# Optimization experiments

Hardware: AMD Instinct MI355X
Metric: run time of the kernel (lower is better)

Reference implementation:

```python
import jax, jax.numpy as jnp
import numpy as np

NUM_SAMPLES = 512
FG_FRACTION = 0.25
MAX_POS = int(NUM_SAMPLES * FG_FRACTION)  # 128
THRESHOLDS = np.array([0.0, 0.5, 0.5], dtype=np.float32)
INDICATORS = np.array([-3, -1, -2, 1], dtype=np.int32)


def _make_boxes(key, shape, scale):
    # random valid boxes: sorted corner pairs in [0, scale)
    y = jnp.sort(jax.random.uniform(key, shape[:-1] + (2,)) * scale, axis=-1)
    x = jnp.sort(jax.random.uniform(jax.random.fold_in(key, 1), shape[:-1] + (2,)) * scale, axis=-1)
    return jnp.stack([y[..., 0], x[..., 0], y[..., 1], x[..., 1]], axis=-1)


def setup_inputs() -> dict:
    key = jax.random.key(0)
    k1, k2, k3, k4 = jax.random.split(key, 4)
    B, N, M = 32, 8000, 256
    boxes = _make_boxes(k1, (B, N, 4), 1024.0)
    gt_boxes = _make_boxes(k2, (B, M, 4), 1024.0)
    # pad last quarter of gt entries with -1 (invalid)
    valid = (jnp.arange(M) < (3 * M) // 4)[None, :, None]
    gt_boxes = jnp.where(valid, gt_boxes, -jnp.ones_like(gt_boxes))
    gt_classes = jax.random.randint(k3, (B, M), 1, 91, dtype=jnp.int32)
    gt_classes = jnp.where(valid[..., 0], gt_classes, -1)
    rand = jax.random.uniform(k4, (B, N + M))
    return {"boxes": boxes, "gt_boxes": gt_boxes, "gt_classes": gt_classes, "rand": rand}


def _pairwise_iou(b1, b2):
    # b1: [B,N,4], b2: [B,M,4] in (ymin,xmin,ymax,xmax) -> [B,N,M]
    ymin1, xmin1, ymax1, xmax1 = jnp.split(b1, 4, axis=-1)  # each [B,N,1]
    ymin2, xmin2, ymax2, xmax2 = (t[..., 0] for t in jnp.split(b2, 4, axis=-1))  # [B,M]
    ih = jnp.clip(jnp.minimum(ymax1, ymax2[:, None, :]) - jnp.maximum(ymin1, ymin2[:, None, :]), 0.0)
    iw = jnp.clip(jnp.minimum(xmax1, xmax2[:, None, :]) - jnp.maximum(xmin1, xmin2[:, None, :]), 0.0)
    inter = ih * iw
    a1 = (ymax1 - ymin1) * (xmax1 - xmin1)          # [B,N,1]
    a2 = (ymax2 - ymin2) * (xmax2 - xmin2)          # [B,M]
    union = a1 + a2[:, None, :] - inter
    return jnp.where(union > 0, inter / union, 0.0)


def _ranks_desc(score):
    order = jnp.argsort(-score)
    return jnp.zeros_like(order).at[order].set(jnp.arange(score.shape[0]))


def _sample_one(pos, neg, ign, rand):
    cand = (pos | neg) & ~ign
    pos_c = pos & cand
    neg_c = neg & cand
    pos_rank = _ranks_desc(jnp.where(pos_c, rand, -1.0))
    pos_sel = pos_c & (pos_rank < MAX_POS)
    neg_needed = NUM_SAMPLES - jnp.sum(pos_sel)
    neg_rank = _ranks_desc(jnp.where(neg_c, rand, -1.0))
    neg_sel = neg_c & (neg_rank < neg_needed)
    indicator = (pos_sel | neg_sel).astype(jnp.int32)
    _, idx = jax.lax.top_k(indicator, NUM_SAMPLES)  # selected first, ties by lowest index
    return idx


def _gather(t, idx):
    # t: [B,L,C], idx: [B,K] -> [B,K,C]
    return jnp.take_along_axis(t, idx[..., None], axis=1)


def reference(boxes, gt_boxes, gt_classes, rand):
    gt_boxes = gt_boxes.astype(boxes.dtype)
    boxes = jnp.concatenate([boxes, gt_boxes], axis=1)  # mix_gt_boxes
    boxes_invalid = jnp.max(boxes, axis=-1) < 0.0       # [B,L]
    gt_invalid = jnp.max(gt_boxes, axis=-1) < 0.0       # [B,M]
    sim = _pairwise_iou(boxes, gt_boxes)                # [B,L,M]
    sim = jnp.where(boxes_invalid[:, :, None] | gt_invalid[:, None, :], -1.0, sim)

    matched_vals = jnp.max(sim, axis=-1)                # [B,L]
    matched_gt_indices = jnp.argmax(sim, axis=-1).astype(jnp.int32)
    bucket = jnp.searchsorted(jnp.asarray(THRESHOLDS), matched_vals, side='right')
    match_indicators = jnp.asarray(INDICATORS)[bucket]  # [B,L]

    positive = match_indicators >= 0
    negative = match_indicators == -1
    ignored = match_indicators == -2
    invalid = match_indicators == -3
    background = negative | invalid                     # [B,L]

    matched_gt_classes = _gather(gt_classes[..., None], matched_gt_indices)[..., 0]
    matched_gt_classes = jnp.where(background, 0, matched_gt_classes)
    matched_gt_boxes = _gather(gt_boxes, matched_gt_indices)
    matched_gt_boxes = jnp.where(background[..., None], 0.0, matched_gt_boxes)
    matched_gt_indices = jnp.where(background, -1, matched_gt_indices)

    indices = jax.vmap(_sample_one)(positive, negative, ignored, rand)  # [B,K]
    rois = _gather(boxes, indices)
    sampled_gt_boxes = _gather(matched_gt_boxes, indices)
    sampled_gt_classes = _gather(matched_gt_classes[..., None], indices)[..., 0]
    sampled_gt_indices = _gather(matched_gt_indices[..., None], indices)[..., 0]
    return rois, sampled_gt_boxes, sampled_gt_classes, sampled_gt_indices
```

## Files before the change

### kernel.cpp

```cpp
#include <hip/hip_runtime.h>
#include <stdint.h>

#define BB 32
#define NN 8000
#define MM 256
#define LL (NN + MM)
#define NSAMP 512
#define MAXPOS 128
#define T2 1024
#define CH ((LL + T2 - 1) / T2)
#define SPLIT 4
#define MSUB (MM / SPLIT)
#define ONE_P 1.0000019073486328f
#define ONE_M 0.9999980926513672f

__device__ __forceinline__ void opaquef(float& x) { asm("" : "+v"(x)); }

__device__ __noinline__ int serial_argmax(const float4 bx, const float a1,
                                          const float4* s_gt, const float* s_a2)
{
    float qb = -1.0f; int bi = 0;
    for (int m = 0; m < MSUB; ++m) {
        float4 g = s_gt[m];
        float ih = fmaxf(fminf(bx.z, g.z) - fmaxf(bx.x, g.x), 0.0f);
        float iw = fmaxf(fminf(bx.w, g.w) - fmaxf(bx.y, g.y), 0.0f);
        float inter = ih * iw; opaquef(inter);
        float uni = (a1 + s_a2[m]) - inter;
        float q = (uni > 0.0f) ? (inter / uni) : 0.0f;
        if (q > qb) { qb = q; bi = m; }
    }
    return bi;
}

__global__ __launch_bounds__(256) void match_split_kernel(
    const float* __restrict__ boxes, const float* __restrict__ gt,
    uint8_t* __restrict__ pidx)
{
    __shared__ float4 s_gt[MSUB];
    __shared__ float  s_a2[MSUB];
    const int b = blockIdx.y, sp = blockIdx.z, tid = threadIdx.x;
    if (tid < MSUB) {
        float4 v = ((const float4*)(gt + ((size_t)b * MM + sp * MSUB) * 4))[tid];
        s_gt[tid] = v;
        s_a2[tid] = (v.z - v.x) * (v.w - v.y);
    }
    __syncthreads();
    const int l0 = blockIdx.x * 512 + tid * 2;
    if (l0 >= LL) return;
    const int l1 = l0 + 1;
    const bool v1 = (l1 < LL);
    const int l1c = v1 ? l1 : l0;

    const float4* bb4 = (const float4*)(boxes + (size_t)b * NN * 4);
    const float4* gb4 = (const float4*)(gt + (size_t)b * MM * 4);
    float4 bx0 = (l0 < NN) ? bb4[l0] : gb4[l0 - NN];
    float4 bx1 = (l1c < NN) ? bb4[l1c] : gb4[l1c - NN];

    float a10 = (bx0.z - bx0.x) * (bx0.w - bx0.y); opaquef(a10);
    float a11 = (bx1.z - bx1.x) * (bx1.w - bx1.y); opaquef(a11);

    float I00 = 0.f, S00 = 1.f, I01 = 0.f, S01 = 1.f;
    float I10 = 0.f, S10 = 1.f, I11 = 0.f, S11 = 1.f;
    int X00 = 0, X01 = 1, X10 = 0, X11 = 1;
    bool redo0 = false, redo1 = false;

    #define STEP(BX, A1, G, A2, BI, BS, BIX, MIDX, RD)                       \
    {                                                                        \
        float ih = fmaxf(fminf(BX.z, G.z) - fmaxf(BX.x, G.x), 0.0f);         \
        float iw = fmaxf(fminf(BX.w, G.w) - fmaxf(BX.y, G.y), 0.0f);         \
        float inter = ih * iw; opaquef(inter);                               \
        float s  = A1 + A2;                                                  \
        float p1 = inter * BS, p2 = BI * s;                                  \
        bool win = p1 > p2 * ONE_P;                                          \
        RD |= ((p1 > p2 * ONE_M) != win);                                    \
        if (win) { BI = inter; BS = s; BIX = MIDX; }                         \
    }
    #pragma unroll 4
    for (int m = 0; m < MSUB; m += 2) {
        float4 g0 = s_gt[m];     float a2_0 = s_a2[m];
        float4 g1 = s_gt[m + 1]; float a2_1 = s_a2[m + 1];
        STEP(bx0, a10, g0, a2_0, I00, S00, X00, m,     redo0)
        STEP(bx0, a10, g1, a2_1, I01, S01, X01, m + 1, redo0)
        STEP(bx1, a11, g0, a2_0, I10, S10, X10, m,     redo1)
        STEP(bx1, a11, g1, a2_1, I11, S11, X11, m + 1, redo1)
    }
    #undef STEP

    #define MERGE(I0, S0, X0, I1, S1, X1, RD)                                \
    {                                                                        \
        float p1 = I1 * S0, p2 = I0 * S1;                                    \
        bool win = p1 > p2 * ONE_P;                                          \
        RD |= ((p1 > p2 * ONE_M) != win);                                    \
        if (win) { X0 = X1; }                                                \
    }
    MERGE(I00, S00, X00, I01, S01, X01, redo0)
    MERGE(I10, S10, X10, I11, S11, X11, redo1)
    #undef MERGE

    int lb0 = X00, lb1 = X10;
    if (__any(redo0 || redo1)) {
        if (redo0) lb0 = serial_argmax(bx0, a10, s_gt, s_a2);
        if (redo1) lb1 = serial_argmax(bx1, a11, s_gt, s_a2);
    }
    pidx[((size_t)b * LL + l0) * SPLIT + sp] = (uint8_t)lb0;
    if (v1) pidx[((size_t)b * LL + l1) * SPLIT + sp] = (uint8_t)lb1;
}

__device__ __forceinline__ int block_exscan_fast(int v, int* wt, int tid)
{
    const int lane = tid & 63, w = tid >> 6;
    int x = v;
    #pragma unroll
    for (int off = 1; off < 64; off <<= 1) {
        int y = __shfl_up(x, off);
        if (lane >= off) x += y;
    }
    if (lane == 63) wt[w] = x;
    __syncthreads();
    if (tid < 64) {
        int t = (tid < 16) ? wt[tid] : 0;
        #pragma unroll
        for (int off = 1; off < 16; off <<= 1) {
            int y = __shfl_up(t, off);
            if (tid >= off) t += y;
        }
        if (tid < 16) wt[tid] = t;
    }
    __syncthreads();
    return ((w > 0) ? wt[w - 1] : 0) + x - v;
}

__device__ __forceinline__ int block_exscan_seg4(int v, int* wt, int tid)
{
    const int lane = tid & 63, w = tid >> 6;
    int x = v;
    #pragma unroll
    for (int off = 1; off < 64; off <<= 1) {
        int y = __shfl_up(x, off);
        if (lane >= off) x += y;
    }
    if (lane == 63) wt[w] = x;
    __syncthreads();
    if (tid < 16) {
        int t = wt[tid];
        #pragma unroll
        for (int off = 1; off < 4; off <<= 1) {
            int y = __shfl_up(t, off);
            if ((tid & 3) >= off) t += y;
        }
        wt[tid] = t;
    }
    __syncthreads();
    return (((w & 3) > 0) ? wt[w - 1] : 0) + x - v;
}

__global__ __launch_bounds__(T2) void sample_kernel(
    const float* __restrict__ boxes, const float* __restrict__ gt,
    const int* __restrict__ gtc, const float* __restrict__ rnd,
    const uint32_t* __restrict__ pidx, float* __restrict__ out)
{
    __shared__ uint32_t s_key[LL];
    __shared__ uint16_t s_pk[LL];
    __shared__ int s_hist[512];
    __shared__ int s_warp[16];
    __shared__ int s_idx[NSAMP];
    __shared__ int s_sb[8];
    const int b = blockIdx.x, tid = threadIdx.x, lane = tid & 63;
    const float4* bb4 = (const float4*)(boxes + (size_t)b * NN * 4);
    const float4* gb4 = (const float4*)(gt + (size_t)b * MM * 4);

    if (tid == 0) s_sb[0] = 0;
    __syncthreads();

    int loc = 0;
    for (int l = tid; l < LL; l += T2) {
        s_key[l] = __float_as_uint(rnd[(size_t)b * LL + l]);
        const uint32_t pv = pidx[(size_t)b * LL + l];
        float4 bx = (l < NN) ? bb4[l] : gb4[l - NN];
        int cls = 2, midx = 0;
        if (!(fmaxf(fmaxf(bx.x, bx.y), fmaxf(bx.z, bx.w)) < 0.0f)) {
            float a1 = (bx.z - bx.x) * (bx.w - bx.y); opaquef(a1);
            float qb = -1.0f;
            #pragma unroll
            for (int sp = 0; sp < SPLIT; ++sp) {
                const int m = sp * MSUB + (int)((pv >> (8 * sp)) & 0xFFu);
                float4 g = gb4[m];
                float a2 = (g.z - g.x) * (g.w - g.y); opaquef(a2);
                float ih = fmaxf(fminf(bx.z, g.z) - fmaxf(bx.x, g.x), 0.0f);
                float iw = fmaxf(fminf(bx.w, g.w) - fmaxf(bx.y, g.y), 0.0f);
                float inter = ih * iw; opaquef(inter);
                float uni = (a1 + a2) - inter;
                float q = (uni > 0.0f) ? (inter / uni) : 0.0f;
                if (q > qb) { qb = q; midx = m; }
            }
            cls = (qb >= 0.5f) ? 1 : 0;
        }
        s_pk[l] = (uint16_t)(cls | (midx << 2));
        loc += (cls == 0) ? 1 : ((cls == 1) ? 0x10000 : 0);
    }
    #pragma unroll
    for (int off = 32; off; off >>= 1) loc += __shfl_xor(loc, off);
    if (lane == 0) atomicAdd(&s_sb[0], loc);
    __syncthreads();
    const int Nn = s_sb[0] & 0xFFFF, P = s_sb[0] >> 16;

    const int posK = (P < MAXPOS) ? P : MAXPOS;
    const int negK = NSAMP - posK;
    const bool negRad = (Nn > negK);
    const bool posRad = (P > MAXPOS);

    uint32_t prefix0 = 0, prefix1 = 0;
    int rem0 = negK, rem1 = MAXPOS;
    if (negRad || posRad) {
        for (int round = 0; round < 4; ++round) {
            const int shift = 24 - 8 * round;
            if (tid < 512) s_hist[tid] = 0;
            __syncthreads();
            const uint32_t pmask = (round == 0) ? 0u : (0xFFFFFFFFu << (shift + 8));
            for (int l = tid; l < LL; l += T2) {
                const uint32_t k = s_key[l];
                const int c = s_pk[l] & 3;
                bool doit = (c == 0) ? (negRad && ((k & pmask) == prefix0))
                          : (c == 1) ? (posRad && ((k & pmask) == prefix1))
                          : false;
                if (doit) atomicAdd(&s_hist[(c << 8) | ((k >> shift) & 255)], 1);
            }
            __syncthreads();
            int h = 0;
            if (tid < 512) h = s_hist[(tid & 0x100) | (255 - (tid & 255))];
            const int above = block_exscan_seg4(h, s_warp, tid);
            if (tid < 512) {
                const int c = tid >> 8;
                const int rem = c ? rem1 : rem0;
                const bool act = c ? posRad : negRad;
                if (act && above < rem && above + h >= rem) {
                    s_sb[4 + c * 2] = 255 - (tid & 255);
                    s_sb[5 + c * 2] = above;
                }
            }
            __syncthreads();
            if (negRad) { prefix0 |= ((uint32_t)s_sb[4]) << shift; rem0 -= s_sb[5]; }
            if (posRad) { prefix1 |= ((uint32_t)s_sb[6]) << shift; rem1 -= s_sb[7]; }
            __syncthreads();
        }
    }
    const uint32_t thr0 = negRad ? prefix0 : 0u;  const int r0 = negRad ? rem0 : LL;
    const uint32_t thr1 = posRad ? prefix1 : 0u;  const int r1 = posRad ? rem1 : LL;

    const int lo = tid * CH, hi = (lo + CH < LL) ? (lo + CH) : LL;
    int nt = 0;
    for (int l = lo; l < hi; ++l) {
        const int c = s_pk[l] & 3;
        const uint32_t k = s_key[l];
        if (c == 0) { if (k == thr0) nt += 1; }
        else if (c == 1) { if (k == thr1) nt += 0x10000; }
    }
    const int basep = block_exscan_fast(nt, s_warp, tid);
    int base0 = basep & 0xFFFF, base1 = basep >> 16;
    for (int l = lo; l < hi; ++l) {
        const int c = s_pk[l] & 3;
        if (c > 1) continue;
        const uint32_t k = s_key[l];
        const uint32_t thr = c ? thr1 : thr0;
        bool sel = (k > thr);
        if (k == thr) {
            if (c == 0) { sel = (base0 < r0); ++base0; }
            else        { sel = (base1 < r1); ++base1; }
        }
        if (sel) s_pk[l] |= 0x8000;
    }
    __syncthreads();

    int cnt = 0;
    for (int l = lo; l < hi; ++l) cnt += (s_pk[l] & 0x8000) ? 1 : 0x10000;
    const int pb = block_exscan_fast(cnt, s_warp, tid);
    const int S = s_warp[15] & 0xFFFF;
    int bs = pb & 0xFFFF, bu = (pb >> 16) + S;
    for (int l = lo; l < hi; ++l) {
        if (s_pk[l] & 0x8000) { if (bs < NSAMP) s_idx[bs] = l; ++bs; }
        else                  { if (bu < NSAMP) s_idx[bu] = l; ++bu; }
    }
    __syncthreads();

    if (tid < NSAMP) {
        const int l = s_idx[tid];
        float4 bx = (l < NN) ? bb4[l] : gb4[l - NN];
        const int p = s_pk[l];
        const int c = p & 3, mi = (p >> 2) & 0xFF;
        const bool bg = (c != 1);
        float4 gb = make_float4(0.f, 0.f, 0.f, 0.f);
        int cl = 0, si = -1;
        if (!bg) {
            gb = gb4[mi];
            cl = gtc[(size_t)b * MM + mi];
            si = mi;
        }
        const size_t rk = (size_t)b * NSAMP + tid;
        ((float4*)out)[rk] = bx;
        ((float4*)(out + (size_t)BB * NSAMP * 4))[rk] = gb;
        out[(size_t)2 * BB * NSAMP * 4 + rk] = (float)cl;
        out[(size_t)2 * BB * NSAMP * 4 + (size_t)BB * NSAMP + rk] = (float)si;
    }
}

extern "C" void kernel_launch(void* const* d_in, const int* in_sizes, int n_in,
                              void* d_out, int out_size, void* d_ws, size_t ws_size,
                              hipStream_t stream)
{
    const float* boxes = (const float*)d_in[0];
    const float* gt    = (const float*)d_in[1];
    const int*   gtc   = (const int*)  d_in[2];
    const float* rnd   = (const float*)d_in[3];
    float* out = (float*)d_out;
    uint8_t* pidx = (uint8_t*)d_ws;

    dim3 g1((LL + 511) / 512, BB, SPLIT);
    match_split_kernel<<<g1, 256, 0, stream>>>(boxes, gt, pidx);
    sample_kernel<<<BB, T2, 0, stream>>>(boxes, gt, gtc, rnd,
                                         (const uint32_t*)d_ws, out);
}
```

Baseline: 74.32 us.

## Combine split-argmax via 64-bit atomicMax keys and early-exit radix select

The match kernel now computes the best IoU per split and combines the splits through a 64-bit atomicMax on a packed key (IoU bits plus an inverted gt index), so the sample kernel no longer re-gathers four gt boxes and recomputes their IoUs per anchor. A memset of the key buffer is added before the match kernel. The radix-select loop in the sample kernel now stops early once the remaining count exactly fills a bin, which skips later histogram rounds. The costs are an extra memset launch, 8-byte atomics to global memory, and a larger workspace footprint.

```diff
diff --git a/kernel.cpp b/kernel.cpp
--- a/kernel.cpp
+++ b/kernel.cpp
@@ -16,8 +16,9 @@
 
 __device__ __forceinline__ void opaquef(float& x) { asm("" : "+v"(x)); }
 
-__device__ __noinline__ int serial_argmax(const float4 bx, const float a1,
-                                          const float4* s_gt, const float* s_a2)
+__device__ __noinline__ void serial_argmax_q(const float4 bx, const float a1,
+                                             const float4* s_gt, const float* s_a2,
+                                             int* obi, float* oq)
 {
     float qb = -1.0f; int bi = 0;
     for (int m = 0; m < MSUB; ++m) {
@@ -29,12 +30,12 @@
         float q = (uni > 0.0f) ? (inter / uni) : 0.0f;
         if (q > qb) { qb = q; bi = m; }
     }
-    return bi;
+    *obi = bi; *oq = qb;
 }
 
 __global__ __launch_bounds__(256) void match_split_kernel(
     const float* __restrict__ boxes, const float* __restrict__ gt,
-    uint8_t* __restrict__ pidx)
+    unsigned long long* __restrict__ keymax)
 {
     __shared__ float4 s_gt[MSUB];
     __shared__ float  s_a2[MSUB];
@@ -55,9 +56,10 @@
     const float4* gb4 = (const float4*)(gt + (size_t)b * MM * 4);
     float4 bx0 = (l0 < NN) ? bb4[l0] : gb4[l0 - NN];
     float4 bx1 = (l1c < NN) ? bb4[l1c] : gb4[l1c - NN];
-
     float a10 = (bx0.z - bx0.x) * (bx0.w - bx0.y); opaquef(a10);
     float a11 = (bx1.z - bx1.x) * (bx1.w - bx1.y); opaquef(a11);
+    const bool binv0 = fmaxf(fmaxf(bx0.x, bx0.y), fmaxf(bx0.z, bx0.w)) < 0.0f;
+    const bool binv1 = fmaxf(fmaxf(bx1.x, bx1.y), fmaxf(bx1.z, bx1.w)) < 0.0f;
 
     float I00 = 0.f, S00 = 1.f, I01 = 0.f, S01 = 1.f;
     float I10 = 0.f, S10 = 1.f, I11 = 0.f, S11 = 1.f;
@@ -91,19 +93,37 @@
         float p1 = I1 * S0, p2 = I0 * S1;                                    \
         bool win = p1 > p2 * ONE_P;                                          \
         RD |= ((p1 > p2 * ONE_M) != win);                                    \
-        if (win) { X0 = X1; }                                                \
+        if (win) { I0 = I1; S0 = S1; X0 = X1; }                              \
     }
     MERGE(I00, S00, X00, I01, S01, X01, redo0)
     MERGE(I10, S10, X10, I11, S11, X11, redo1)
     #undef MERGE
 
-    int lb0 = X00, lb1 = X10;
+    float q0, q1; int m0 = X00, m1 = X10;
     if (__any(redo0 || redo1)) {
-        if (redo0) lb0 = serial_argmax(bx0, a10, s_gt, s_a2);
-        if (redo1) lb1 = serial_argmax(bx1, a11, s_gt, s_a2);
-    }
-    pidx[((size_t)b * LL + l0) * SPLIT + sp] = (uint8_t)lb0;
-    if (v1) pidx[((size_t)b * LL + l1) * SPLIT + sp] = (uint8_t)lb1;
+        if (redo0) serial_argmax_q(bx0, a10, s_gt, s_a2, &m0, &q0);
+        if (redo1) serial_argmax_q(bx1, a11, s_gt, s_a2, &m1, &q1);
+    }
+    if (!redo0) {
+        float uni = S00 - I00;
+        q0 = (uni > 0.0f) ? (I00 / uni) : 0.0f;
+    }
+    if (!redo1) {
+        float uni = S10 - I10;
+        q1 = (uni > 0.0f) ? (I10 / uni) : 0.0f;
+    }
+    if (!binv0) {
+        unsigned long long key =
+            (((unsigned long long)(__float_as_uint(q0) + 1u)) << 32)
+            | (unsigned long long)(255 - (sp * MSUB + m0));
+        atomicMax(&keymax[(size_t)b * LL + l0], key);
+    }
+    if (v1 && !binv1) {
+        unsigned long long key =
+            (((unsigned long long)(__float_as_uint(q1) + 1u)) << 32)
+            | (unsigned long long)(255 - (sp * MSUB + m1));
+        atomicMax(&keymax[(size_t)b * LL + l1], key);
+    }
 }
 
 __device__ __forceinline__ int block_exscan_fast(int v, int* wt, int tid)
@@ -157,7 +177,7 @@
 __global__ __launch_bounds__(T2) void sample_kernel(
     const float* __restrict__ boxes, const float* __restrict__ gt,
     const int* __restrict__ gtc, const float* __restrict__ rnd,
-    const uint32_t* __restrict__ pidx, float* __restrict__ out)
+    const unsigned long long* __restrict__ keymax, float* __restrict__ out)
 {
     __shared__ uint32_t s_key[LL];
     __shared__ uint16_t s_pk[LL];
@@ -175,28 +195,19 @@
     int loc = 0;
     for (int l = tid; l < LL; l += T2) {
         s_key[l] = __float_as_uint(rnd[(size_t)b * LL + l]);
-        const uint32_t pv = pidx[(size_t)b * LL + l];
-        float4 bx = (l < NN) ? bb4[l] : gb4[l - NN];
-        int cls = 2, midx = 0;
-        if (!(fmaxf(fmaxf(bx.x, bx.y), fmaxf(bx.z, bx.w)) < 0.0f)) {
-            float a1 = (bx.z - bx.x) * (bx.w - bx.y); opaquef(a1);
-            float qb = -1.0f;
-            #pragma unroll
-            for (int sp = 0; sp < SPLIT; ++sp) {
-                const int m = sp * MSUB + (int)((pv >> (8 * sp)) & 0xFFu);
-                float4 g = gb4[m];
-                float a2 = (g.z - g.x) * (g.w - g.y); opaquef(a2);
-                float ih = fmaxf(fminf(bx.z, g.z) - fmaxf(bx.x, g.x), 0.0f);
-                float iw = fmaxf(fminf(bx.w, g.w) - fmaxf(bx.y, g.y), 0.0f);
-                float inter = ih * iw; opaquef(inter);
-                float uni = (a1 + a2) - inter;
-                float q = (uni > 0.0f) ? (inter / uni) : 0.0f;
-                if (q > qb) { qb = q; midx = m; }
-            }
-            cls = (qb >= 0.5f) ? 1 : 0;
-        }
-        s_pk[l] = (uint16_t)(cls | (midx << 2));
-        loc += (cls == 0) ? 1 : ((cls == 1) ? 0x10000 : 0);
+        const unsigned long long kk = keymax[(size_t)b * LL + l];
+        uint16_t p;
+        if (kk == 0ull) {
+            p = 2;
+        } else {
+            const uint32_t qb = (uint32_t)(kk >> 32) - 1u;
+            const int gidx = 255 - (int)(kk & 0xFFull);
+            const int cls = (qb >= 0x3F000000u) ? 1 : 0;
+            p = (uint16_t)(cls | (gidx << 2));
+        }
+        s_pk[l] = p;
+        int c = p & 3;
+        loc += (c == 0) ? 1 : ((c == 1) ? 0x10000 : 0);
     }
     #pragma unroll
     for (int off = 32; off; off >>= 1) loc += __shfl_xor(loc, off);
@@ -211,41 +222,56 @@
 
     uint32_t prefix0 = 0, prefix1 = 0;
     int rem0 = negK, rem1 = MAXPOS;
-    if (negRad || posRad) {
-        for (int round = 0; round < 4; ++round) {
-            const int shift = 24 - 8 * round;
-            if (tid < 512) s_hist[tid] = 0;
-            __syncthreads();
-            const uint32_t pmask = (round == 0) ? 0u : (0xFFFFFFFFu << (shift + 8));
-            for (int l = tid; l < LL; l += T2) {
-                const uint32_t k = s_key[l];
-                const int c = s_pk[l] & 3;
-                bool doit = (c == 0) ? (negRad && ((k & pmask) == prefix0))
-                          : (c == 1) ? (posRad && ((k & pmask) == prefix1))
-                          : false;
-                if (doit) atomicAdd(&s_hist[(c << 8) | ((k >> shift) & 255)], 1);
+    bool act0 = negRad, act1 = posRad;
+    uint32_t thr0f = 0, thr1f = 0;
+    int r0f = LL, r1f = LL;
+    for (int round = 0; round < 4 && (act0 || act1); ++round) {
+        const int shift = 24 - 8 * round;
+        if (tid < 512) s_hist[tid] = 0;
+        __syncthreads();
+        const uint32_t pmask = (round == 0) ? 0u : (0xFFFFFFFFu << (shift + 8));
+        for (int l = tid; l < LL; l += T2) {
+            const uint32_t k = s_key[l];
+            const int c = s_pk[l] & 3;
+            bool doit = (c == 0) ? (act0 && ((k & pmask) == prefix0))
+                      : (c == 1) ? (act1 && ((k & pmask) == prefix1))
+                      : false;
+            if (doit) atomicAdd(&s_hist[(c << 8) | ((k >> shift) & 255)], 1);
+        }
+        __syncthreads();
+        int h = 0;
+        if (tid < 512) h = s_hist[(tid & 0x100) | (255 - (tid & 255))];
+        const int above = block_exscan_seg4(h, s_warp, tid);
+        if (tid < 512) {
+            const int c = tid >> 8;
+            const int rem = c ? rem1 : rem0;
+            const bool act = c ? act1 : act0;
+            if (act && above < rem && above + h >= rem) {
+                s_sb[4 + c * 2] = 255 - (tid & 255);
+                s_sb[5 + c * 2] = above;
             }
-            __syncthreads();
-            int h = 0;
-            if (tid < 512) h = s_hist[(tid & 0x100) | (255 - (tid & 255))];
-            const int above = block_exscan_seg4(h, s_warp, tid);
-            if (tid < 512) {
-                const int c = tid >> 8;
-                const int rem = c ? rem1 : rem0;
-                const bool act = c ? posRad : negRad;
-                if (act && above < rem && above + h >= rem) {
-                    s_sb[4 + c * 2] = 255 - (tid & 255);
-                    s_sb[5 + c * 2] = above;
-                }
-            }
-            __syncthreads();
-            if (negRad) { prefix0 |= ((uint32_t)s_sb[4]) << shift; rem0 -= s_sb[5]; }
-            if (posRad) { prefix1 |= ((uint32_t)s_sb[6]) << shift; rem1 -= s_sb[7]; }
-            __syncthreads();
-        }
-    }
-    const uint32_t thr0 = negRad ? prefix0 : 0u;  const int r0 = negRad ? rem0 : LL;
-    const uint32_t thr1 = posRad ? prefix1 : 0u;  const int r1 = posRad ? rem1 : LL;
+        }
+        __syncthreads();
+        if (act0) {
+            const int bin = s_sb[4];
+            rem0 -= s_sb[5];
+            prefix0 |= ((uint32_t)bin) << shift;
+            const int cnt = s_hist[bin];
+            if (rem0 == cnt)      { act0 = false; thr0f = prefix0; r0f = LL; }
+            else if (round == 3)  { act0 = false; thr0f = prefix0; r0f = rem0; }
+        }
+        if (act1) {
+            const int bin = s_sb[6];
+            rem1 -= s_sb[7];
+            prefix1 |= ((uint32_t)bin) << shift;
+            const int cnt = s_hist[256 + bin];
+            if (rem1 == cnt)      { act1 = false; thr1f = prefix1; r1f = LL; }
+            else if (round == 3)  { act1 = false; thr1f = prefix1; r1f = rem1; }
+        }
+        __syncthreads();
+    }
+    const uint32_t thr0 = negRad ? thr0f : 0u;  const int r0 = negRad ? r0f : LL;
+    const uint32_t thr1 = posRad ? thr1f : 0u;  const int r1 = posRad ? r1f : LL;
 
     const int lo = tid * CH, hi = (lo + CH < LL) ? (lo + CH) : LL;
     int nt = 0;
@@ -312,10 +338,10 @@
     const int*   gtc   = (const int*)  d_in[2];
     const float* rnd   = (const float*)d_in[3];
     float* out = (float*)d_out;
-    uint8_t* pidx = (uint8_t*)d_ws;
-
+    unsigned long long* keymax = (unsigned long long*)d_ws;
+
+    hipMemsetAsync(d_ws, 0, (size_t)BB * LL * 8, stream);
     dim3 g1((LL + 511) / 512, BB, SPLIT);
-    match_split_kernel<<<g1, 256, 0, stream>>>(boxes, gt, pidx);
-    sample_kernel<<<BB, T2, 0, stream>>>(boxes, gt, gtc, rnd,
-                                         (const uint32_t*)d_ws, out);
-}
+    match_split_kernel<<<g1, 256, 0, stream>>>(boxes, gt, keymax);
+    sample_kernel<<<BB, T2, 0, stream>>>(boxes, gt, gtc, rnd, keymax, out);
+}
```

After: 73.02 us. Within noise of the previous version (-1.7%).

## Move IoU merge into separate wide kernel and exit radix select early

Applied to the files above, without the earlier changes.

The per-element IoU recomputation that merges the four split argmax candidates moves out of the 32-block sample kernel into a new grid-wide merge kernel. The merge kernel writes a packed class/index array, and the sample kernel only loads it. This spreads work that was confined to 32 blocks across the whole GPU, at the cost of an extra launch and a global round trip. The radix select also stops early once the remaining count exactly fills the selected bin, skipping the later histogram rounds.

```diff
diff --git a/kernel.cpp b/kernel.cpp
--- a/kernel.cpp
+++ b/kernel.cpp
@@ -106,6 +106,39 @@
     if (v1) pidx[((size_t)b * LL + l1) * SPLIT + sp] = (uint8_t)lb1;
 }
 
+__global__ __launch_bounds__(256) void merge_kernel(
+    const float* __restrict__ boxes, const float* __restrict__ gt,
+    const uint8_t* __restrict__ pidx, uint16_t* __restrict__ packed)
+{
+    const int b = blockIdx.y;
+    const int l = blockIdx.x * 256 + threadIdx.x;
+    if (l >= LL) return;
+    float4 bx = (l < NN) ? ((const float4*)(boxes + (size_t)b * NN * 4))[l]
+                         : ((const float4*)(gt + (size_t)b * MM * 4))[l - NN];
+    int cls, bidx = 0;
+    if (fmaxf(fmaxf(bx.x, bx.y), fmaxf(bx.z, bx.w)) < 0.0f) {
+        cls = 2;
+    } else {
+        float a1 = (bx.z - bx.x) * (bx.w - bx.y); opaquef(a1);
+        float qb = -1.0f;
+        const uint32_t pv = *(const uint32_t*)&pidx[((size_t)b * LL + l) * SPLIT];
+        #pragma unroll
+        for (int sp = 0; sp < SPLIT; ++sp) {
+            const int m = sp * MSUB + (int)((pv >> (8 * sp)) & 0xFFu);
+            float4 g = ((const float4*)(gt + (size_t)b * MM * 4))[m];
+            float a2 = (g.z - g.x) * (g.w - g.y); opaquef(a2);
+            float ih = fmaxf(fminf(bx.z, g.z) - fmaxf(bx.x, g.x), 0.0f);
+            float iw = fmaxf(fminf(bx.w, g.w) - fmaxf(bx.y, g.y), 0.0f);
+            float inter = ih * iw; opaquef(inter);
+            float uni = (a1 + a2) - inter;
+            float q = (uni > 0.0f) ? (inter / uni) : 0.0f;
+            if (q > qb) { qb = q; bidx = m; }
+        }
+        cls = (qb >= 0.5f) ? 1 : 0;
+    }
+    packed[(size_t)b * LL + l] = (uint16_t)(cls | (bidx << 2));
+}
+
 __device__ __forceinline__ int block_exscan_fast(int v, int* wt, int tid)
 {
     const int lane = tid & 63, w = tid >> 6;
@@ -157,7 +190,7 @@
 __global__ __launch_bounds__(T2) void sample_kernel(
     const float* __restrict__ boxes, const float* __restrict__ gt,
     const int* __restrict__ gtc, const float* __restrict__ rnd,
-    const uint32_t* __restrict__ pidx, float* __restrict__ out)
+    const uint16_t* __restrict__ packed, float* __restrict__ out)
 {
     __shared__ uint32_t s_key[LL];
     __shared__ uint16_t s_pk[LL];
@@ -175,28 +208,10 @@
     int loc = 0;
     for (int l = tid; l < LL; l += T2) {
         s_key[l] = __float_as_uint(rnd[(size_t)b * LL + l]);
-        const uint32_t pv = pidx[(size_t)b * LL + l];
-        float4 bx = (l < NN) ? bb4[l] : gb4[l - NN];
-        int cls = 2, midx = 0;
-        if (!(fmaxf(fmaxf(bx.x, bx.y), fmaxf(bx.z, bx.w)) < 0.0f)) {
-            float a1 = (bx.z - bx.x) * (bx.w - bx.y); opaquef(a1);
-            float qb = -1.0f;
-            #pragma unroll
-            for (int sp = 0; sp < SPLIT; ++sp) {
-                const int m = sp * MSUB + (int)((pv >> (8 * sp)) & 0xFFu);
-                float4 g = gb4[m];
-                float a2 = (g.z - g.x) * (g.w - g.y); opaquef(a2);
-                float ih = fmaxf(fminf(bx.z, g.z) - fmaxf(bx.x, g.x), 0.0f);
-                float iw = fmaxf(fminf(bx.w, g.w) - fmaxf(bx.y, g.y), 0.0f);
-                float inter = ih * iw; opaquef(inter);
-                float uni = (a1 + a2) - inter;
-                float q = (uni > 0.0f) ? (inter / uni) : 0.0f;
-                if (q > qb) { qb = q; midx = m; }
-            }
-            cls = (qb >= 0.5f) ? 1 : 0;
-        }
-        s_pk[l] = (uint16_t)(cls | (midx << 2));
-        loc += (cls == 0) ? 1 : ((cls == 1) ? 0x10000 : 0);
+        uint16_t p = packed[(size_t)b * LL + l];
+        s_pk[l] = p;
+        int c = p & 3;
+        loc += (c == 0) ? 1 : ((c == 1) ? 0x10000 : 0);
     }
     #pragma unroll
     for (int off = 32; off; off >>= 1) loc += __shfl_xor(loc, off);
@@ -211,41 +226,56 @@
 
     uint32_t prefix0 = 0, prefix1 = 0;
     int rem0 = negK, rem1 = MAXPOS;
-    if (negRad || posRad) {
-        for (int round = 0; round < 4; ++round) {
-            const int shift = 24 - 8 * round;
-            if (tid < 512) s_hist[tid] = 0;
-            __syncthreads();
-            const uint32_t pmask = (round == 0) ? 0u : (0xFFFFFFFFu << (shift + 8));
-            for (int l = tid; l < LL; l += T2) {
-                const uint32_t k = s_key[l];
-                const int c = s_pk[l] & 3;
-                bool doit = (c == 0) ? (negRad && ((k & pmask) == prefix0))
-                          : (c == 1) ? (posRad && ((k & pmask) == prefix1))
-                          : false;
-                if (doit) atomicAdd(&s_hist[(c << 8) | ((k >> shift) & 255)], 1);
+    bool act0 = negRad, act1 = posRad;
+    uint32_t thr0f = 0, thr1f = 0;
+    int r0f = LL, r1f = LL;
+    for (int round = 0; round < 4 && (act0 || act1); ++round) {
+        const int shift = 24 - 8 * round;
+        if (tid < 512) s_hist[tid] = 0;
+        __syncthreads();
+        const uint32_t pmask = (round == 0) ? 0u : (0xFFFFFFFFu << (shift + 8));
+        for (int l = tid; l < LL; l += T2) {
+            const uint32_t k = s_key[l];
+            const int c = s_pk[l] & 3;
+            bool doit = (c == 0) ? (act0 && ((k & pmask) == prefix0))
+                      : (c == 1) ? (act1 && ((k & pmask) == prefix1))
+                      : false;
+            if (doit) atomicAdd(&s_hist[(c << 8) | ((k >> shift) & 255)], 1);
+        }
+        __syncthreads();
+        int h = 0;
+        if (tid < 512) h = s_hist[(tid & 0x100) | (255 - (tid & 255))];
+        const int above = block_exscan_seg4(h, s_warp, tid);
+        if (tid < 512) {
+            const int c = tid >> 8;
+            const int rem = c ? rem1 : rem0;
+            const bool act = c ? act1 : act0;
+            if (act && above < rem && above + h >= rem) {
+                s_sb[4 + c * 2] = 255 - (tid & 255);
+                s_sb[5 + c * 2] = above;
             }
-            __syncthreads();
-            int h = 0;
-            if (tid < 512) h = s_hist[(tid & 0x100) | (255 - (tid & 255))];
-            const int above = block_exscan_seg4(h, s_warp, tid);
-            if (tid < 512) {
-                const int c = tid >> 8;
-                const int rem = c ? rem1 : rem0;
-                const bool act = c ? posRad : negRad;
-                if (act && above < rem && above + h >= rem) {
-                    s_sb[4 + c * 2] = 255 - (tid & 255);
-                    s_sb[5 + c * 2] = above;
-                }
-            }
-            __syncthreads();
-            if (negRad) { prefix0 |= ((uint32_t)s_sb[4]) << shift; rem0 -= s_sb[5]; }
-            if (posRad) { prefix1 |= ((uint32_t)s_sb[6]) << shift; rem1 -= s_sb[7]; }
-            __syncthreads();
-        }
-    }
-    const uint32_t thr0 = negRad ? prefix0 : 0u;  const int r0 = negRad ? rem0 : LL;
-    const uint32_t thr1 = posRad ? prefix1 : 0u;  const int r1 = posRad ? rem1 : LL;
+        }
+        __syncthreads();
+        if (act0) {
+            const int bin = s_sb[4];
+            rem0 -= s_sb[5];
+            prefix0 |= ((uint32_t)bin) << shift;
+            const int cnt = s_hist[bin];
+            if (rem0 == cnt)      { act0 = false; thr0f = prefix0; r0f = LL; }
+            else if (round == 3)  { act0 = false; thr0f = prefix0; r0f = rem0; }
+        }
+        if (act1) {
+            const int bin = s_sb[6];
+            rem1 -= s_sb[7];
+            prefix1 |= ((uint32_t)bin) << shift;
+            const int cnt = s_hist[256 + bin];
+            if (rem1 == cnt)      { act1 = false; thr1f = prefix1; r1f = LL; }
+            else if (round == 3)  { act1 = false; thr1f = prefix1; r1f = rem1; }
+        }
+        __syncthreads();
+    }
+    const uint32_t thr0 = negRad ? thr0f : 0u;  const int r0 = negRad ? r0f : LL;
+    const uint32_t thr1 = posRad ? thr1f : 0u;  const int r1 = posRad ? r1f : LL;
 
     const int lo = tid * CH, hi = (lo + CH < LL) ? (lo + CH) : LL;
     int nt = 0;
@@ -312,10 +342,12 @@
     const int*   gtc   = (const int*)  d_in[2];
     const float* rnd   = (const float*)d_in[3];
     float* out = (float*)d_out;
-    uint8_t* pidx = (uint8_t*)d_ws;
+    uint8_t*  pidx   = (uint8_t*)d_ws;
+    uint16_t* packed = (uint16_t*)((char*)d_ws + (size_t)BB * LL * SPLIT);
 
     dim3 g1((LL + 511) / 512, BB, SPLIT);
     match_split_kernel<<<g1, 256, 0, stream>>>(boxes, gt, pidx);
-    sample_kernel<<<BB, T2, 0, stream>>>(boxes, gt, gtc, rnd,
-                                         (const uint32_t*)d_ws, out);
-}
+    dim3 g2((LL + 255) / 256, BB);
+    merge_kernel<<<g2, 256, 0, stream>>>(boxes, gt, pidx, packed);
+    sample_kernel<<<BB, T2, 0, stream>>>(boxes, gt, gtc, rnd, packed, out);
+}
```

Measured after the change: 68.02 us. 1.09x faster.
